# Optimization experiments

Measured on AMD Instinct MI355X. Metric: run time of the kernel, lower is better.

The kernel has to match this reference:

```python
import jax, jax.numpy as jnp
import numpy as np

B, S, D = 1, 2048, 2048
H, KVH = 32, 8
HD = D // H          # 64
N_REP = H // KVH     # 4
ROPE_THETA = 10000.0
NEG = -1e9


def setup_inputs() -> dict:
    key = jax.random.key(0)
    ks = jax.random.split(key, 8)
    x = jax.random.normal(ks[0], (B, S, D), dtype=jnp.float32)
    # RoPE tables: freqs_cis[t, j] = exp(i * t * theta^{-2j/HD}), j in [0, HD/2)
    inv_freq = 1.0 / (ROPE_THETA ** (jnp.arange(0, HD, 2, dtype=jnp.float32) / HD))
    angles = jnp.arange(S, dtype=jnp.float32)[:, None] * inv_freq[None, :]  # (S, HD/2)
    freqs_cos = jnp.cos(angles)
    freqs_sin = jnp.sin(angles)
    # causal additive mask (S, S)
    mask = jnp.where(jnp.tril(jnp.ones((S, S), dtype=bool)), 0.0, NEG).astype(jnp.float32)
    sc = 0.02
    wq = jax.random.normal(ks[1], (D, H * HD), dtype=jnp.float32) * sc
    wk = jax.random.normal(ks[2], (D, KVH * HD), dtype=jnp.float32) * sc
    wv = jax.random.normal(ks[3], (D, KVH * HD), dtype=jnp.float32) * sc
    wo = jax.random.normal(ks[4], (H * HD, D), dtype=jnp.float32) * sc
    fw = jax.random.normal(ks[5], (HD, HD), dtype=jnp.float32) * sc
    fb = jnp.zeros((HD,), dtype=jnp.float32)
    return {"x": x, "freqs_cos": freqs_cos, "freqs_sin": freqs_sin, "mask": mask,
            "wq": wq, "wk": wk, "wv": wv, "wo": wo, "fw": fw, "fb": fb,
            "start_pos": 0}


def _rope(t, cos, sin):
    # t: (B, S, h, HD) -> complex rotate pairs along last dim
    tr = t.reshape(*t.shape[:-1], HD // 2, 2)
    c = cos[None, :, None, :]  # (1, S, 1, HD/2)
    s = sin[None, :, None, :]
    re = tr[..., 0] * c - tr[..., 1] * s
    im = tr[..., 0] * s + tr[..., 1] * c
    return jnp.stack([re, im], axis=-1).reshape(t.shape)


def reference(x, freqs_cos, freqs_sin, mask, wq, wk, wv, wo, fw, fb, start_pos):
    b, s, _ = x.shape
    xq = (x @ wq).reshape(b, s, H, HD)
    xk = (x @ wk).reshape(b, s, KVH, HD)
    xv = (x @ wv).reshape(b, s, KVH, HD)
    xq = _rope(xq, freqs_cos, freqs_sin)
    xk = _rope(xk, freqs_cos, freqs_sin)
    # GQA: repeat kv heads (repeat_interleave on head dim)
    keys = jnp.repeat(xk, N_REP, axis=2)    # (b, s, H, HD)
    values = jnp.repeat(xv, N_REP, axis=2)
    q = xq.transpose(0, 2, 1, 3)            # (b, H, s, HD)
    k = keys.transpose(0, 2, 1, 3)
    v = values.transpose(0, 2, 1, 3)
    scores = jnp.einsum("bhqd,bhkd->bhqk", q, k) / np.sqrt(HD).astype(np.float32)
    scores = scores + mask[None, None, :, :]
    probs = jax.nn.softmax(scores.astype(jnp.float32), axis=-1).astype(q.dtype)
    out = jnp.einsum("bhqk,bhkd->bhqd", probs, v)  # (b, H, s, HD)
    # shared per-head FFN: Linear(HD, HD) + SiLU, vectorized over heads
    out = jax.nn.silu(out @ fw + fb)
    out = out.transpose(0, 2, 1, 3).reshape(b, s, H * HD)
    return out @ wo
```

## Files before the change

kernel.cpp:

```cpp
#include <hip/hip_runtime.h>
#include <stdint.h>

#define S_LEN 2048
#define DMODEL 2048
#define NH 32
#define NKV 8
#define HD 64

typedef __attribute__((ext_vector_type(8))) __bf16 bf16x8;
typedef __attribute__((ext_vector_type(4))) float f32x4;
typedef __attribute__((ext_vector_type(16))) float f32x16;

__device__ __forceinline__ unsigned short f2bf(float f) {
    union { float f; uint32_t u; } v; v.f = f;
    uint32_t u = v.u;
    u += 0x7FFFu + ((u >> 16) & 1u);
    return (unsigned short)(u >> 16);
}

__device__ __forceinline__ uint32_t cvt_pk_bf16(float lo, float hi) {
    uint32_t r;
    asm("v_cvt_pk_bf16_f32 %0, %1, %2" : "=v"(r) : "v"(lo), "v"(hi));
    return r;
}

#define GLDS16(g, l)                                                          \
    __builtin_amdgcn_global_load_lds(                                         \
        (const __attribute__((address_space(1))) unsigned int*)(g),           \
        (__attribute__((address_space(3))) unsigned int*)(l), 16, 0, 0)

__global__ void cast_bf16_kernel(const float* __restrict__ src,
                                 unsigned short* __restrict__ dst, int n) {
    int g = (blockIdx.x * blockDim.x + threadIdx.x) * 8;
    if (g >= n) return;
    float4 a = *(const float4*)&src[g];
    float4 b = *(const float4*)&src[g + 4];
    unsigned short o[8];
    o[0] = f2bf(a.x); o[1] = f2bf(a.y); o[2] = f2bf(a.z); o[3] = f2bf(a.w);
    o[4] = f2bf(b.x); o[5] = f2bf(b.y); o[6] = f2bf(b.z); o[7] = f2bf(b.w);
    *(uint4*)&dst[g] = *(const uint4*)o;
}

__global__ void transpose_cast_kernel(const float* __restrict__ src,
                                      unsigned short* __restrict__ dst,
                                      int R, int C) {
    __shared__ float tile[32][33];
    int c0 = blockIdx.x * 32, r0 = blockIdx.y * 32;
    int tx = threadIdx.x, ty = threadIdx.y;
#pragma unroll
    for (int i = 0; i < 32; i += 8)
        tile[ty + i][tx] = src[(size_t)(r0 + ty + i) * C + c0 + tx];
    __syncthreads();
#pragma unroll
    for (int i = 0; i < 32; i += 8)
        dst[(size_t)(c0 + ty + i) * R + r0 + tx] = f2bf(tile[tx][ty + i]);
}

__global__ __launch_bounds__(256) void gemm_bt_kernel(
    const unsigned short* __restrict__ A, const unsigned short* __restrict__ BT,
    float* __restrict__ C0, float* __restrict__ C1, int M, int N,
    int Kstride, int Klen) {
    __shared__ unsigned short As[2][128 * 32];
    __shared__ unsigned short Bs[2][128 * 32];
    const int t = threadIdx.x;
    const int lane = t & 63, wave = t >> 6;
    const int wr = wave >> 1, wc = wave & 1;
    const int m0 = blockIdx.x * 128, n0 = blockIdx.y * 128;
    const int koff = blockIdx.z * Klen;
    float* __restrict__ C = blockIdx.z ? C1 : C0;
    const int l15 = lane & 15, lhi = lane >> 4;
    f32x4 acc[4][4] = {};
    const unsigned short* ga = A + (size_t)(m0 + (t >> 2)) * Kstride + koff + (t & 3) * 8;
    const unsigned short* gb = BT + (size_t)(n0 + (t >> 2)) * Kstride + koff + (t & 3) * 8;

    GLDS16(ga, &As[0][t * 8]);
    GLDS16(ga + (size_t)64 * Kstride, &As[0][t * 8 + 64 * 32]);
    GLDS16(gb, &Bs[0][t * 8]);
    GLDS16(gb + (size_t)64 * Kstride, &Bs[0][t * 8 + 64 * 32]);
    __syncthreads();

    int cur = 0;
    for (int k0 = 0; k0 < Klen; k0 += 32) {
        if (k0 + 32 < Klen) {
            GLDS16(ga + k0 + 32, &As[cur ^ 1][t * 8]);
            GLDS16(ga + (size_t)64 * Kstride + k0 + 32, &As[cur ^ 1][t * 8 + 64 * 32]);
            GLDS16(gb + k0 + 32, &Bs[cur ^ 1][t * 8]);
            GLDS16(gb + (size_t)64 * Kstride + k0 + 32, &Bs[cur ^ 1][t * 8 + 64 * 32]);
        }
        bf16x8 af[4], bfr[4];
#pragma unroll
        for (int m = 0; m < 4; m++)
            af[m] = *(const bf16x8*)&As[cur][(wr * 64 + m * 16 + l15) * 32 + lhi * 8];
#pragma unroll
        for (int n = 0; n < 4; n++)
            bfr[n] = *(const bf16x8*)&Bs[cur][(wc * 64 + n * 16 + l15) * 32 + lhi * 8];
#pragma unroll
        for (int m = 0; m < 4; m++)
#pragma unroll
            for (int n = 0; n < 4; n++)
                acc[m][n] = __builtin_amdgcn_mfma_f32_16x16x32_bf16(
                    af[m], bfr[n], acc[m][n], 0, 0, 0);
        __syncthreads();
        cur ^= 1;
    }
#pragma unroll
    for (int m = 0; m < 4; m++) {
        int row = m0 + wr * 64 + m * 16 + lhi * 4;
#pragma unroll
        for (int n = 0; n < 4; n++) {
            int col = n0 + wc * 64 + n * 16 + l15;
#pragma unroll
            for (int r = 0; r < 4; r++)
                C[(size_t)(row + r) * N + col] = acc[m][n][r];
        }
    }
}

__global__ void add_f32_kernel(float* __restrict__ out,
                               const float* __restrict__ p1, int n4) {
    int g = blockIdx.x * blockDim.x + threadIdx.x;
    if (g >= n4) return;
    float4 a = *(const float4*)&out[g * 4];
    float4 b = *(const float4*)&p1[g * 4];
    a.x += b.x; a.y += b.y; a.z += b.z; a.w += b.w;
    *(float4*)&out[g * 4] = a;
}

__global__ void rope_q_kernel(const float* __restrict__ Cqkv,
                              const float* __restrict__ cb,
                              const float* __restrict__ sb,
                              unsigned short* __restrict__ Q) {
    const float CS = 0.125f * 1.44269504f;
    int g = blockIdx.x * 256 + threadIdx.x;
    int i = g & 31;
    int h = (g >> 5) & 31;
    int s = g >> 10;
    float2 v = *(const float2*)&Cqkv[(size_t)s * 3072 + h * 64 + 2 * i];
    float cc = cb[s * 32 + i], ss = sb[s * 32 + i];
    ushort2 o;
    o.x = f2bf((v.x * cc - v.y * ss) * CS);
    o.y = f2bf((v.x * ss + v.y * cc) * CS);
    *(ushort2*)&Q[(size_t)h * (S_LEN * HD) + s * HD + 2 * i] = o;
}

__global__ void rope_k_kernel(const float* __restrict__ Cqkv,
                              const float* __restrict__ cb,
                              const float* __restrict__ sb,
                              unsigned short* __restrict__ Kb) {
    int g = blockIdx.x * 256 + threadIdx.x;
    int i = g & 31;
    int kvh = (g >> 5) & 7;
    int s = g >> 8;
    float2 v = *(const float2*)&Cqkv[(size_t)s * 3072 + 2048 + kvh * 64 + 2 * i];
    float cc = cb[s * 32 + i], ss = sb[s * 32 + i];
    ushort2 o;
    o.x = f2bf(v.x * cc - v.y * ss);
    o.y = f2bf(v.x * ss + v.y * cc);
    *(ushort2*)&Kb[(size_t)kvh * (S_LEN * HD) + s * HD + 2 * i] = o;
}

__global__ void v_transpose_kernel(const float* __restrict__ Cqkv,
                                   unsigned short* __restrict__ VT) {
    __shared__ float tile[32][33];
    int kvh = blockIdx.z;
    int d0 = blockIdx.x * 32, s0 = blockIdx.y * 32;
    int tx = threadIdx.x, ty = threadIdx.y;
#pragma unroll
    for (int i = 0; i < 32; i += 8)
        tile[ty + i][tx] =
            Cqkv[(size_t)(s0 + ty + i) * 3072 + 2560 + kvh * 64 + d0 + tx];
    __syncthreads();
#pragma unroll
    for (int i = 0; i < 32; i += 8)
        VT[(size_t)kvh * (HD * S_LEN) + (size_t)(d0 + ty + i) * S_LEN + s0 + tx] =
            f2bf(tile[tx][ty + i]);
}

__global__ __launch_bounds__(256) void flash_kernel(
    const unsigned short* __restrict__ Q, const unsigned short* __restrict__ Kg,
    const unsigned short* __restrict__ VTg, unsigned short* __restrict__ O) {
    __shared__ unsigned short Ks[3][4096];
    __shared__ unsigned short Vs[3][4096];
    const int t = threadIdx.x, lane = t & 63, wave = t >> 6;
    const int l31 = lane & 31, hi = lane >> 5;
    const int bid = blockIdx.x;
    const int h = bid & 31, ss = bid >> 5;
    const int qt = (ss < 8) ? (15 - ss) : (ss - 8);
    const int kvh = h >> 2;

    const int srow = t >> 3;
    const int scol = ((t & 7) * 8) ^ ((srow & 7) * 8);
    const unsigned short* gk = Kg + ((size_t)kvh * S_LEN + srow) * HD + scol;
    const unsigned short* gv = VTg + ((size_t)kvh * HD + srow) * S_LEN + scol;

    const int q0 = qt * 128;
    const int nt = 2 * qt + 2;
    const int qw0 = q0 + wave * 32;
    const int q = qw0 + l31;

    const unsigned short* qp = Q + ((size_t)h * S_LEN + q) * HD + hi * 8;
    bf16x8 qf0 = *(const bf16x8*)(qp);
    bf16x8 qf1 = *(const bf16x8*)(qp + 16);
    bf16x8 qf2 = *(const bf16x8*)(qp + 32);
    bf16x8 qf3 = *(const bf16x8*)(qp + 48);

    f32x16 oacc0 = {}, oacc1 = {};
    float mrun = -1e30f, lrun = 0.f;

    GLDS16(gk, &Ks[0][t * 8]);
    GLDS16(gk + (size_t)32 * HD, &Ks[0][t * 8 + 2048]);
    GLDS16(gv, &Vs[0][t * 8]);
    GLDS16(gv + (size_t)32 * S_LEN, &Vs[0][t * 8 + 2048]);
    GLDS16(gk + (size_t)64 * HD, &Ks[1][t * 8]);
    GLDS16(gk + (size_t)96 * HD, &Ks[1][t * 8 + 2048]);
    GLDS16(gv + 64, &Vs[1][t * 8]);
    GLDS16(gv + (size_t)32 * S_LEN + 64, &Vs[1][t * 8 + 2048]);

#pragma unroll 1
    for (int kt = 0; kt < nt; ++kt) {
        if (kt + 1 < nt) asm volatile("s_waitcnt vmcnt(4)" ::: "memory");
        else             asm volatile("s_waitcnt vmcnt(0)" ::: "memory");
        __builtin_amdgcn_s_barrier();
        __builtin_amdgcn_sched_barrier(0);
        if (kt + 2 < nt) {
            const int pb = (kt + 2) % 3;
            const size_t kvp = (size_t)(kt + 2) * 64;
            GLDS16(gk + kvp * HD, &Ks[pb][t * 8]);
            GLDS16(gk + (kvp + 32) * HD, &Ks[pb][t * 8 + 2048]);
            GLDS16(gv + kvp, &Vs[pb][t * 8]);
            GLDS16(gv + (size_t)32 * S_LEN + kvp, &Vs[pb][t * 8 + 2048]);
        }
        const int kv0 = kt * 64;
        if (kv0 > qw0 + 31) continue;
        const int cb = kt % 3;
        const unsigned short* ksb = Ks[cb];
        const unsigned short* vsb = Vs[cb];
        const int sw = (l31 & 7) * 8;
        f32x16 s0 = {}, s1 = {};
#pragma unroll
        for (int kc = 0; kc < 4; kc++) {
            bf16x8 k0 = *(const bf16x8*)&ksb[l31 * 64 + ((16 * kc + 8 * hi) ^ sw)];
            bf16x8 k1 = *(const bf16x8*)&ksb[(32 + l31) * 64 + ((16 * kc + 8 * hi) ^ sw)];
            bf16x8 qc = (kc == 0) ? qf0 : (kc == 1) ? qf1 : (kc == 2) ? qf2 : qf3;
            s0 = __builtin_amdgcn_mfma_f32_32x32x16_bf16(k0, qc, s0, 0, 0, 0);
            s1 = __builtin_amdgcn_mfma_f32_32x32x16_bf16(k1, qc, s1, 0, 0, 0);
        }
        float p0[16], p1[16];
        if (kv0 + 63 <= qw0) {
#pragma unroll
            for (int r = 0; r < 16; r++) { p0[r] = s0[r]; p1[r] = s1[r]; }
        } else {
#pragma unroll
            for (int r = 0; r < 16; r++) {
                int rr = (r & 3) + 8 * (r >> 2) + 4 * hi;
                p0[r] = (kv0 + rr <= q) ? s0[r] : -1e30f;
                p1[r] = (kv0 + 32 + rr <= q) ? s1[r] : -1e30f;
            }
        }
        float t8[8];
#pragma unroll
        for (int r = 0; r < 8; r++)
            t8[r] = fmaxf(fmaxf(p0[r], p0[r + 8]), fmaxf(p1[r], p1[r + 8]));
        float lm = fmaxf(fmaxf(fmaxf(t8[0], t8[4]), fmaxf(t8[1], t8[5])),
                         fmaxf(fmaxf(t8[2], t8[6]), fmaxf(t8[3], t8[7])));
        if (!__all(lm - mrun <= 8.f)) {
            float rm = fmaxf(lm, __shfl_xor(lm, 32));
            float mnew = fmaxf(mrun, rm);
            float sc = exp2f(mrun - mnew);
            mrun = mnew;
            lrun *= sc;
            oacc0 *= sc;
            oacc1 *= sc;
        }
#pragma unroll
        for (int r = 0; r < 16; r++) {
            p0[r] = exp2f(p0[r] - mrun);
            p1[r] = exp2f(p1[r] - mrun);
        }
        float sA = 0.f, sB = 0.f, sC = 0.f, sD = 0.f;
#pragma unroll
        for (int r = 0; r < 4; r++) {
            sA += p0[r] + p1[r];
            sB += p0[r + 4] + p1[r + 4];
            sC += p0[r + 8] + p1[r + 8];
            sD += p0[r + 12] + p1[r + 12];
        }
        lrun += (sA + sB) + (sC + sD);
        bf16x8 pf[4];
#pragma unroll
        for (int kc = 0; kc < 4; kc++) {
            const int sub = (kc & 1) * 8;
            uint32_t Wl0, Wl1, Wh0, Wh1;
            if (kc < 2) {
                Wl0 = cvt_pk_bf16(p0[sub + 0], p0[sub + 1]);
                Wl1 = cvt_pk_bf16(p0[sub + 2], p0[sub + 3]);
                Wh0 = cvt_pk_bf16(p0[sub + 4], p0[sub + 5]);
                Wh1 = cvt_pk_bf16(p0[sub + 6], p0[sub + 7]);
            } else {
                Wl0 = cvt_pk_bf16(p1[sub + 0], p1[sub + 1]);
                Wl1 = cvt_pk_bf16(p1[sub + 2], p1[sub + 3]);
                Wh0 = cvt_pk_bf16(p1[sub + 4], p1[sub + 5]);
                Wh1 = cvt_pk_bf16(p1[sub + 6], p1[sub + 7]);
            }
            uint32_t sw0 = hi ? Wl0 : Wh0, sw1 = hi ? Wl1 : Wh1;
            uint32_t rc0 = __shfl_xor((int)sw0, 32);
            uint32_t rc1 = __shfl_xor((int)sw1, 32);
            uint32_t kp0 = hi ? Wh0 : Wl0, kp1 = hi ? Wh1 : Wl1;
            uint32_t F0 = hi ? rc0 : kp0;
            uint32_t F1 = hi ? rc1 : kp1;
            uint32_t F2 = hi ? kp0 : rc0;
            uint32_t F3 = hi ? kp1 : rc1;
            uint4 fu = {F0, F1, F2, F3};
            pf[kc] = *(const bf16x8*)&fu;
        }
#pragma unroll
        for (int kc = 0; kc < 4; kc++) {
            bf16x8 v0 = *(const bf16x8*)&vsb[l31 * 64 + ((16 * kc + 8 * hi) ^ sw)];
            bf16x8 v1 = *(const bf16x8*)&vsb[(32 + l31) * 64 + ((16 * kc + 8 * hi) ^ sw)];
            oacc0 = __builtin_amdgcn_mfma_f32_32x32x16_bf16(v0, pf[kc], oacc0, 0, 0, 0);
            oacc1 = __builtin_amdgcn_mfma_f32_32x32x16_bf16(v1, pf[kc], oacc1, 0, 0, 0);
        }
    }
    lrun += __shfl_xor(lrun, 32);
    float rinv = 1.f / lrun;
    unsigned short* ob = O + ((size_t)h * S_LEN + q) * HD + 4 * hi;
#pragma unroll
    for (int g = 0; g < 4; g++) {
        uint32_t a0 = cvt_pk_bf16(oacc0[4 * g] * rinv, oacc0[4 * g + 1] * rinv);
        uint32_t a1 = cvt_pk_bf16(oacc0[4 * g + 2] * rinv, oacc0[4 * g + 3] * rinv);
        uint2 u0 = {a0, a1};
        *(uint2*)(ob + 8 * g) = u0;
        uint32_t b0 = cvt_pk_bf16(oacc1[4 * g] * rinv, oacc1[4 * g + 1] * rinv);
        uint32_t b1 = cvt_pk_bf16(oacc1[4 * g + 2] * rinv, oacc1[4 * g + 3] * rinv);
        uint2 u1 = {b0, b1};
        *(uint2*)(ob + 32 + 8 * g) = u1;
    }
}

__global__ __launch_bounds__(256) void fw_silu_kernel(
    const unsigned short* __restrict__ AT, const unsigned short* __restrict__ fwT,
    const float* __restrict__ fb, unsigned short* __restrict__ h2) {
    const int t = threadIdx.x, lane = t & 63, wave = t >> 6;
    const int l15 = lane & 15, lhi = lane >> 4;
    const int r0 = blockIdx.x * 64 + wave * 16;
    const unsigned short* ap = AT + (size_t)(r0 + l15) * HD + lhi * 8;
    bf16x8 a0 = *(const bf16x8*)ap;
    bf16x8 a1 = *(const bf16x8*)(ap + 32);
    f32x4 acc[4] = {};
#pragma unroll
    for (int nb = 0; nb < 4; nb++) {
        const unsigned short* bp = fwT + (size_t)(nb * 16 + l15) * HD + lhi * 8;
        bf16x8 b0 = *(const bf16x8*)bp;
        bf16x8 b1 = *(const bf16x8*)(bp + 32);
        acc[nb] = __builtin_amdgcn_mfma_f32_16x16x32_bf16(a0, b0, acc[nb], 0, 0, 0);
        acc[nb] = __builtin_amdgcn_mfma_f32_16x16x32_bf16(a1, b1, acc[nb], 0, 0, 0);
    }
#pragma unroll
    for (int nb = 0; nb < 4; nb++) {
        int col = nb * 16 + l15;
        float bias = fb[col];
#pragma unroll
        for (int r = 0; r < 4; r++) {
            int row = r0 + lhi * 4 + r;
            int s = row & (S_LEN - 1), hh = row >> 11;
            float x = acc[nb][r] + bias;
            float sg = 1.f / (1.f + exp2f(-x * 1.44269504f));
            h2[(size_t)s * DMODEL + hh * HD + col] = f2bf(x * sg);
        }
    }
}

extern "C" void kernel_launch(void* const* d_in, const int* in_sizes, int n_in,
                              void* d_out, int out_size, void* d_ws, size_t ws_size,
                              hipStream_t stream) {
    const float* x = (const float*)d_in[0];
    const float* fcos = (const float*)d_in[1];
    const float* fsin = (const float*)d_in[2];
    const float* wq = (const float*)d_in[4];
    const float* wk = (const float*)d_in[5];
    const float* wv = (const float*)d_in[6];
    const float* wo = (const float*)d_in[7];
    const float* fw = (const float*)d_in[8];
    const float* fb = (const float*)d_in[9];
    float* out = (float*)d_out;

    char* ws = (char*)d_ws;
    size_t off = 0;
    auto alloc = [&](size_t bytes) {
        void* p = ws + off;
        off += (bytes + 255) & ~(size_t)255;
        return p;
    };
    unsigned short* wqkvT = (unsigned short*)alloc((size_t)3072 * 2048 * 2);
    unsigned short* woT   = (unsigned short*)alloc((size_t)2048 * 2048 * 2);
    unsigned short* fwT   = (unsigned short*)alloc((size_t)64 * 64 * 2);
    float*          Cqkv  = (float*)alloc((size_t)2048 * 3072 * 4);
    unsigned short* Qb    = (unsigned short*)alloc((size_t)NH * S_LEN * HD * 2);
    unsigned short* Kb    = (unsigned short*)alloc((size_t)NKV * S_LEN * HD * 2);
    unsigned short* VT    = (unsigned short*)alloc((size_t)NKV * HD * S_LEN * 2);
    unsigned short* xb    = (unsigned short*)alloc((size_t)2048 * 2048 * 2);
    unsigned short* attn = (unsigned short*)Cqkv;
    float* P1 = (float*)((char*)Cqkv + (size_t)NH * S_LEN * HD * 2);
    unsigned short* h2 = xb;

    dim3 tb(32, 8);
    cast_bf16_kernel<<<2048, 256, 0, stream>>>(x, xb, 2048 * 2048);
    transpose_cast_kernel<<<dim3(64, 64), tb, 0, stream>>>(wq, wqkvT, 2048, 2048);
    transpose_cast_kernel<<<dim3(16, 64), tb, 0, stream>>>(wk, wqkvT + (size_t)2048 * 2048, 2048, 512);
    transpose_cast_kernel<<<dim3(16, 64), tb, 0, stream>>>(wv, wqkvT + (size_t)2560 * 2048, 2048, 512);
    transpose_cast_kernel<<<dim3(64, 64), tb, 0, stream>>>(wo, woT, 2048, 2048);
    transpose_cast_kernel<<<dim3(2, 2), tb, 0, stream>>>(fw, fwT, 64, 64);

    gemm_bt_kernel<<<dim3(16, 24, 1), 256, 0, stream>>>(xb, wqkvT, Cqkv, nullptr,
                                                        2048, 3072, 2048, 2048);

    rope_q_kernel<<<8192, 256, 0, stream>>>(Cqkv, fcos, fsin, Qb);
    rope_k_kernel<<<2048, 256, 0, stream>>>(Cqkv, fcos, fsin, Kb);
    v_transpose_kernel<<<dim3(2, 64, 8), tb, 0, stream>>>(Cqkv, VT);

    flash_kernel<<<512, 256, 0, stream>>>(Qb, Kb, VT, attn);

    fw_silu_kernel<<<1024, 256, 0, stream>>>(attn, fwT, fb, h2);

    gemm_bt_kernel<<<dim3(16, 16, 2), 256, 0, stream>>>(h2, woT, out, P1,
                                                        2048, 2048, 2048, 1024);
    add_f32_kernel<<<4096, 256, 0, stream>>>(out, P1, 1048576);
}
```

Baseline: 194.3 us.

## Split long causal query tiles across two blocks and merge with combine kernel

The flash attention grid grows from 512 to 768 blocks. Query tiles 8–15, which carry the most KV work under the causal mask, are each split into two KV-range chunks. A lookup table orders the work units so that big and small units are interleaved for load balance. Split chunks write unnormalized fp32 partial outputs plus running max and sum, and a new combine kernel merges them and writes bf16. This trades an extra kernel launch and fp32 partial traffic for a shorter critical path and better CU balance.

```diff
diff --git a/kernel.cpp b/kernel.cpp
--- a/kernel.cpp
+++ b/kernel.cpp
@@ -28,6 +28,10 @@
     __builtin_amdgcn_global_load_lds(                                         \
         (const __attribute__((address_space(1))) unsigned int*)(g),           \
         (__attribute__((address_space(3))) unsigned int*)(l), 16, 0, 0)
+
+__device__ const int kUQT[24] = {15,15,7,14,14,13,13,6,12,12,11,11,5,10,10,9,9,4,8,8,3,2,1,0};
+__device__ const int kUCH[24] = {0,1,0,0,1,0,1,0,0,1,0,1,0,0,1,0,1,0,0,1,0,0,0,0};
+__device__ const int kUSP[24] = {1,1,0,1,1,1,1,0,1,1,1,1,0,1,1,1,1,0,1,1,0,0,0,0};
 
 __global__ void cast_bf16_kernel(const float* __restrict__ src,
                                  unsigned short* __restrict__ dst, int n) {
@@ -178,15 +182,19 @@
 
 __global__ __launch_bounds__(256) void flash_kernel(
     const unsigned short* __restrict__ Q, const unsigned short* __restrict__ Kg,
-    const unsigned short* __restrict__ VTg, unsigned short* __restrict__ O) {
+    const unsigned short* __restrict__ VTg, unsigned short* __restrict__ O,
+    float* __restrict__ Opart, float* __restrict__ ML) {
     __shared__ unsigned short Ks[3][4096];
     __shared__ unsigned short Vs[3][4096];
     const int t = threadIdx.x, lane = t & 63, wave = t >> 6;
     const int l31 = lane & 31, hi = lane >> 5;
     const int bid = blockIdx.x;
-    const int h = bid & 31, ss = bid >> 5;
-    const int qt = (ss < 8) ? (15 - ss) : (ss - 8);
+    const int h = bid & 31, u = bid >> 5;
+    const int qt = kUQT[u], ch = kUCH[u], sp = kUSP[u];
     const int kvh = h >> 2;
+
+    const int kt0 = sp ? ch * (qt + 1) : 0;
+    const int ktN = sp ? kt0 + qt + 1 : 2 * qt + 2;
 
     const int srow = t >> 3;
     const int scol = ((t & 7) * 8) ^ ((srow & 7) * 8);
@@ -194,7 +202,6 @@
     const unsigned short* gv = VTg + ((size_t)kvh * HD + srow) * S_LEN + scol;
 
     const int q0 = qt * 128;
-    const int nt = 2 * qt + 2;
     const int qw0 = q0 + wave * 32;
     const int q = qw0 + l31;
 
@@ -207,34 +214,39 @@
     f32x16 oacc0 = {}, oacc1 = {};
     float mrun = -1e30f, lrun = 0.f;
 
-    GLDS16(gk, &Ks[0][t * 8]);
-    GLDS16(gk + (size_t)32 * HD, &Ks[0][t * 8 + 2048]);
-    GLDS16(gv, &Vs[0][t * 8]);
-    GLDS16(gv + (size_t)32 * S_LEN, &Vs[0][t * 8 + 2048]);
-    GLDS16(gk + (size_t)64 * HD, &Ks[1][t * 8]);
-    GLDS16(gk + (size_t)96 * HD, &Ks[1][t * 8 + 2048]);
-    GLDS16(gv + 64, &Vs[1][t * 8]);
-    GLDS16(gv + (size_t)32 * S_LEN + 64, &Vs[1][t * 8 + 2048]);
-
+    {
+        const size_t kva = (size_t)kt0 * 64, kvb = kva + 64;
+        GLDS16(gk + kva * HD, &Ks[0][t * 8]);
+        GLDS16(gk + (kva + 32) * HD, &Ks[0][t * 8 + 2048]);
+        GLDS16(gv + kva, &Vs[0][t * 8]);
+        GLDS16(gv + (size_t)32 * S_LEN + kva, &Vs[0][t * 8 + 2048]);
+        GLDS16(gk + kvb * HD, &Ks[1][t * 8]);
+        GLDS16(gk + (kvb + 32) * HD, &Ks[1][t * 8 + 2048]);
+        GLDS16(gv + kvb, &Vs[1][t * 8]);
+        GLDS16(gv + (size_t)32 * S_LEN + kvb, &Vs[1][t * 8 + 2048]);
+    }
+
+    int cb = 0, pfb = 2;
 #pragma unroll 1
-    for (int kt = 0; kt < nt; ++kt) {
-        if (kt + 1 < nt) asm volatile("s_waitcnt vmcnt(4)" ::: "memory");
-        else             asm volatile("s_waitcnt vmcnt(0)" ::: "memory");
+    for (int kt = kt0; kt < ktN; ++kt) {
+        if (kt + 1 < ktN) asm volatile("s_waitcnt vmcnt(4)" ::: "memory");
+        else              asm volatile("s_waitcnt vmcnt(0)" ::: "memory");
         __builtin_amdgcn_s_barrier();
         __builtin_amdgcn_sched_barrier(0);
-        if (kt + 2 < nt) {
-            const int pb = (kt + 2) % 3;
+        if (kt + 2 < ktN) {
             const size_t kvp = (size_t)(kt + 2) * 64;
-            GLDS16(gk + kvp * HD, &Ks[pb][t * 8]);
-            GLDS16(gk + (kvp + 32) * HD, &Ks[pb][t * 8 + 2048]);
-            GLDS16(gv + kvp, &Vs[pb][t * 8]);
-            GLDS16(gv + (size_t)32 * S_LEN + kvp, &Vs[pb][t * 8 + 2048]);
-        }
+            GLDS16(gk + kvp * HD, &Ks[pfb][t * 8]);
+            GLDS16(gk + (kvp + 32) * HD, &Ks[pfb][t * 8 + 2048]);
+            GLDS16(gv + kvp, &Vs[pfb][t * 8]);
+            GLDS16(gv + (size_t)32 * S_LEN + kvp, &Vs[pfb][t * 8 + 2048]);
+        }
+        pfb = (pfb == 2) ? 0 : pfb + 1;
         const int kv0 = kt * 64;
+        const int mycb = cb;
+        cb = (cb == 2) ? 0 : cb + 1;
         if (kv0 > qw0 + 31) continue;
-        const int cb = kt % 3;
-        const unsigned short* ksb = Ks[cb];
-        const unsigned short* vsb = Vs[cb];
+        const unsigned short* ksb = Ks[mycb];
+        const unsigned short* vsb = Vs[mycb];
         const int sw = (l31 & 7) * 8;
         f32x16 s0 = {}, s1 = {};
 #pragma unroll
@@ -322,18 +334,71 @@
         }
     }
     lrun += __shfl_xor(lrun, 32);
-    float rinv = 1.f / lrun;
-    unsigned short* ob = O + ((size_t)h * S_LEN + q) * HD + 4 * hi;
-#pragma unroll
-    for (int g = 0; g < 4; g++) {
-        uint32_t a0 = cvt_pk_bf16(oacc0[4 * g] * rinv, oacc0[4 * g + 1] * rinv);
-        uint32_t a1 = cvt_pk_bf16(oacc0[4 * g + 2] * rinv, oacc0[4 * g + 3] * rinv);
-        uint2 u0 = {a0, a1};
-        *(uint2*)(ob + 8 * g) = u0;
-        uint32_t b0 = cvt_pk_bf16(oacc1[4 * g] * rinv, oacc1[4 * g + 1] * rinv);
-        uint32_t b1 = cvt_pk_bf16(oacc1[4 * g + 2] * rinv, oacc1[4 * g + 3] * rinv);
-        uint2 u1 = {b0, b1};
-        *(uint2*)(ob + 32 + 8 * g) = u1;
+    const int qrow = wave * 32 + l31;
+    if (sp) {
+        const int pidx = (h * 8 + (qt - 8)) * 2 + ch;
+        float* po = Opart + ((size_t)pidx * 128 + qrow) * 64 + 4 * hi;
+#pragma unroll
+        for (int g = 0; g < 4; g++) {
+            float4 a = {oacc0[4 * g], oacc0[4 * g + 1], oacc0[4 * g + 2], oacc0[4 * g + 3]};
+            *(float4*)(po + 8 * g) = a;
+            float4 b = {oacc1[4 * g], oacc1[4 * g + 1], oacc1[4 * g + 2], oacc1[4 * g + 3]};
+            *(float4*)(po + 32 + 8 * g) = b;
+        }
+        if (hi == 0) {
+            ML[((size_t)pidx * 128 + qrow) * 2] = mrun;
+            ML[((size_t)pidx * 128 + qrow) * 2 + 1] = lrun;
+        }
+    } else {
+        float rinv = 1.f / lrun;
+        unsigned short* ob = O + ((size_t)h * S_LEN + q) * HD + 4 * hi;
+#pragma unroll
+        for (int g = 0; g < 4; g++) {
+            uint32_t a0 = cvt_pk_bf16(oacc0[4 * g] * rinv, oacc0[4 * g + 1] * rinv);
+            uint32_t a1 = cvt_pk_bf16(oacc0[4 * g + 2] * rinv, oacc0[4 * g + 3] * rinv);
+            uint2 u0 = {a0, a1};
+            *(uint2*)(ob + 8 * g) = u0;
+            uint32_t b0 = cvt_pk_bf16(oacc1[4 * g] * rinv, oacc1[4 * g + 1] * rinv);
+            uint32_t b1 = cvt_pk_bf16(oacc1[4 * g + 2] * rinv, oacc1[4 * g + 3] * rinv);
+            uint2 u1 = {b0, b1};
+            *(uint2*)(ob + 32 + 8 * g) = u1;
+        }
+    }
+}
+
+__global__ __launch_bounds__(256) void flash_combine_kernel(
+    const float* __restrict__ Opart, const float* __restrict__ ML,
+    unsigned short* __restrict__ attn) {
+    const int bid = blockIdx.x;
+    const int h = bid & 31, j = bid >> 5;
+    const int qt = 8 + j;
+    const int t = threadIdx.x;
+    const int qrow = t >> 1, d0 = (t & 1) * 32;
+    const int base = (h * 8 + j) * 2;
+    const float mA = ML[((size_t)base * 128 + qrow) * 2];
+    const float lA = ML[((size_t)base * 128 + qrow) * 2 + 1];
+    const float mB = ML[((size_t)(base + 1) * 128 + qrow) * 2];
+    const float lB = ML[((size_t)(base + 1) * 128 + qrow) * 2 + 1];
+    const float m = fmaxf(mA, mB);
+    const float wA = exp2f(mA - m), wB = exp2f(mB - m);
+    const float rinv = 1.f / (lA * wA + lB * wB);
+    const float* pA = Opart + ((size_t)base * 128 + qrow) * 64 + d0;
+    const float* pB = Opart + ((size_t)(base + 1) * 128 + qrow) * 64 + d0;
+    unsigned short* po = attn + ((size_t)h * S_LEN + qt * 128 + qrow) * HD + d0;
+#pragma unroll
+    for (int dd = 0; dd < 32; dd += 8) {
+        float4 a0 = *(const float4*)&pA[dd], a1 = *(const float4*)&pA[dd + 4];
+        float4 b0 = *(const float4*)&pB[dd], b1 = *(const float4*)&pB[dd + 4];
+        unsigned short o[8];
+        o[0] = f2bf((a0.x * wA + b0.x * wB) * rinv);
+        o[1] = f2bf((a0.y * wA + b0.y * wB) * rinv);
+        o[2] = f2bf((a0.z * wA + b0.z * wB) * rinv);
+        o[3] = f2bf((a0.w * wA + b0.w * wB) * rinv);
+        o[4] = f2bf((a1.x * wA + b1.x * wB) * rinv);
+        o[5] = f2bf((a1.y * wA + b1.y * wB) * rinv);
+        o[6] = f2bf((a1.z * wA + b1.z * wB) * rinv);
+        o[7] = f2bf((a1.w * wA + b1.w * wB) * rinv);
+        *(uint4*)&po[dd] = *(const uint4*)o;
     }
 }
 
@@ -399,8 +464,10 @@
     unsigned short* Kb    = (unsigned short*)alloc((size_t)NKV * S_LEN * HD * 2);
     unsigned short* VT    = (unsigned short*)alloc((size_t)NKV * HD * S_LEN * 2);
     unsigned short* xb    = (unsigned short*)alloc((size_t)2048 * 2048 * 2);
+    float*          ML    = (float*)alloc((size_t)512 * 128 * 2 * 4);
     unsigned short* attn = (unsigned short*)Cqkv;
     float* P1 = (float*)((char*)Cqkv + (size_t)NH * S_LEN * HD * 2);
+    float* Opart = P1;
     unsigned short* h2 = xb;
 
     dim3 tb(32, 8);
@@ -418,7 +485,8 @@
     rope_k_kernel<<<2048, 256, 0, stream>>>(Cqkv, fcos, fsin, Kb);
     v_transpose_kernel<<<dim3(2, 64, 8), tb, 0, stream>>>(Cqkv, VT);
 
-    flash_kernel<<<512, 256, 0, stream>>>(Qb, Kb, VT, attn);
+    flash_kernel<<<768, 256, 0, stream>>>(Qb, Kb, VT, attn, Opart, ML);
+    flash_combine_kernel<<<256, 256, 0, stream>>>(Opart, ML, attn);
 
     fw_silu_kernel<<<1024, 256, 0, stream>>>(attn, fwT, fb, h2);
 
```

After: 193.1 us. No clear change (-0.6%).
